# Kernel optimization log

Measured on AMD Instinct MI355X. Metric: run time of the kernel, lower is better.

Reference implementation:

```python
import jax, jax.numpy as jnp
import numpy as np

B, T, C, H = 2, 1024, 1024, 16
D = C // H                      # head_dim = 64
NG, BS = 64, 16                 # HBS groups / block_size (1024 = 64*16)
SQ = 32                         # sqrt_dim (1024 = 32*32)


def layer_norm(x, g, b, eps=1e-5):
    m = jnp.mean(x, axis=-1, keepdims=True)
    v = jnp.var(x, axis=-1, keepdims=True)
    return (x - m) * jax.lax.rsqrt(v + eps) * g + b


def hbs_proj(x, pre_g, pre_b, block_w, w_row, w_col, alpha, bias):
    # HierarchicalBlockShuffleLayer forward (dim=1024, no padding needed)
    xn = layer_norm(x, pre_g, pre_b)
    x_flat = xn.reshape(-1, C)
    # block mixing: per-group 16x16 matmul, then flip feature axis
    g = x_flat.reshape(-1, NG, BS)
    y_mixed = jnp.einsum('ngi,gij->ngj', g, block_w).reshape(-1, C)
    block_out = y_mixed[..., ::-1]
    # monarch branch: 32x32 grid, right-multiply W_col then W_row^T
    grid = x_flat.reshape(-1, SQ, SQ)
    z = jnp.einsum('nij,jc->nic', grid, w_col)
    z = jnp.einsum('nic,rc->nir', z, w_row).reshape(-1, C)
    out = block_out + alpha * z + bias
    return out.reshape(x.shape)


def setup_inputs() -> dict:
    key = jax.random.key(0)
    ks = jax.random.split(key, 12)
    inp = {
        'x': jax.random.normal(ks[0], (B, T, C), jnp.float32),
        'c_attn_w': jax.random.normal(ks[1], (3 * C, C), jnp.float32) * (1.0 / np.sqrt(C)),
        'c_attn_b': jnp.zeros((3 * C,), jnp.float32),
        'focus_gate': jnp.float32(0.0),
        'attn_norm_g': jnp.ones((D,), jnp.float32),
        'attn_norm_b': jnp.zeros((D,), jnp.float32),
        'out_norm_g': jnp.ones((C,), jnp.float32),
        'out_norm_b': jnp.zeros((C,), jnp.float32),
        'proj_pre_g': jnp.ones((C,), jnp.float32),
        'proj_pre_b': jnp.zeros((C,), jnp.float32),
        'proj_block_w': jax.random.normal(ks[2], (NG, BS, BS), jnp.float32) * 0.5 / np.sqrt(BS),
        'proj_w_row': jax.random.normal(ks[3], (SQ, SQ), jnp.float32) * 0.1 / np.sqrt(SQ),
        'proj_w_col': jax.random.normal(ks[4], (SQ, SQ), jnp.float32) * 0.1 / np.sqrt(SQ),
        'proj_alpha': jnp.float32(0.0),
        'proj_bias': jnp.zeros((C,), jnp.float32),
    }
    return inp


def reference(x, c_attn_w, c_attn_b, focus_gate, attn_norm_g, attn_norm_b,
              out_norm_g, out_norm_b, proj_pre_g, proj_pre_b, proj_block_w,
              proj_w_row, proj_w_col, proj_alpha, proj_bias):
    scale = 1.0 / np.sqrt(D)
    qkv = x @ c_attn_w.T + c_attn_b                      # [B,T,3C]
    q, k, v = jnp.split(qkv, 3, axis=2)
    # [B,H,T,D]
    q = q.reshape(B, T, H, D).transpose(0, 2, 1, 3)
    k = k.reshape(B, T, H, D).transpose(0, 2, 1, 3)
    v = v.reshape(B, T, H, D).transpose(0, 2, 1, 3)

    # --- causal linear attention branch (fp32) ---
    Qp = jax.nn.elu(q * scale) + 1.0
    Kp = jax.nn.elu(k * scale) + 1.0
    KV = jnp.einsum('bhtd,bhte->bhtde', Kp, v)           # [B,H,T,D,D]
    KV_cum = jnp.cumsum(KV, axis=2)
    K_cum = jnp.cumsum(Kp, axis=2)
    numer = jnp.einsum('bhtd,bhtde->bhte', Qp, KV_cum)
    denom = jnp.einsum('bhtd,bhtd->bht', Qp, K_cum)[..., None]
    y_lin = numer / (denom + 1e-4)                       # [B,H,T,D]
    y_lin = layer_norm(y_lin.transpose(0, 2, 1, 3), attn_norm_g, attn_norm_b)
    y_lin = y_lin.transpose(0, 2, 1, 3)

    # --- standard causal SDPA branch ---
    scores = jnp.einsum('bhqd,bhkd->bhqk', q, k) * scale
    causal = jnp.tril(jnp.ones((T, T), bool))
    scores = jnp.where(causal, scores, -jnp.inf)
    attn = jax.nn.softmax(scores, axis=-1)
    y_sharp = jnp.einsum('bhqk,bhkd->bhqd', attn, v)

    # --- gated combine + output projection ---
    alpha = jax.nn.sigmoid(focus_gate)
    y = alpha * y_sharp + (1.0 - alpha) * y_lin
    y = y.transpose(0, 2, 1, 3).reshape(B, T, C)
    y = layer_norm(y, out_norm_g, out_norm_b)
    return hbs_proj(y, proj_pre_g, proj_pre_b, proj_block_w,
                    proj_w_row, proj_w_col, proj_alpha, proj_bias)
```

## Files before the change

kernel.cpp:

```cpp
#include <hip/hip_runtime.h>
#include <math.h>

constexpr int T_ = 1024;
constexpr int C_ = 1024;
constexpr int H_ = 16;
constexpr int D_ = 64;
#define SCALE 0.125f

typedef unsigned short u16;
typedef __attribute__((ext_vector_type(8))) short short8;
typedef __attribute__((ext_vector_type(4))) float f32x4;

__device__ __forceinline__ float elu1(float x) { return x > 0.f ? x + 1.f : expf(x); }

__device__ __forceinline__ u16 f2bf(float f) {
    union { float f; unsigned u; } c; c.f = f;
    unsigned r = (c.u + 0x7fffu + ((c.u >> 16) & 1u)) >> 16;
    return (u16)r;
}
__device__ __forceinline__ float bf2f(u16 u) {
    union { unsigned u; float f; } c; c.u = (unsigned)u << 16;
    return c.f;
}

#define GLL16(g, l)                                                            \
    __builtin_amdgcn_global_load_lds(                                          \
        (const __attribute__((address_space(1))) void*)(g),                    \
        (__attribute__((address_space(3))) void*)(l), 16, 0, 0)

__global__ __launch_bounds__(256) void k0_cast(
    const float* __restrict__ s, u16* __restrict__ d, int n4)
{
    int i = blockIdx.x * 256 + threadIdx.x;
    if (i < n4) {
        float4 v = reinterpret_cast<const float4*>(s)[i];
        ushort4 o;
        o.x = f2bf(v.x); o.y = f2bf(v.y); o.z = f2bf(v.z); o.w = f2bf(v.w);
        reinterpret_cast<ushort4*>(d)[i] = o;
    }
}

__global__ __launch_bounds__(256) void k1_qkv(
    const u16* __restrict__ xbf, const u16* __restrict__ wbf,
    const float* __restrict__ bias,
    u16* __restrict__ qb, u16* __restrict__ kb, u16* __restrict__ vb)
{
    __shared__ __align__(16) u16 As[128 * 32];
    __shared__ __align__(16) u16 Bs[128 * 32];
    const int tid = threadIdx.x;
    const int wave = tid >> 6, lane = tid & 63;
    const int quad = lane >> 4, l15 = lane & 15;
    const int m0 = blockIdx.y << 7, n0 = blockIdx.x << 7;
    const int wm = (wave >> 1) << 6, wn = (wave & 1) << 6;

    const int rowS = (wave << 5) + (lane >> 2);
    const int seg8 = (lane & 3) << 3;
    const u16* gA1 = xbf + (size_t)(m0 + rowS) * 1024 + seg8;
    const u16* gA2 = gA1 + (size_t)16 * 1024;
    const u16* gB1 = wbf + (size_t)(n0 + rowS) * 1024 + seg8;
    const u16* gB2 = gB1 + (size_t)16 * 1024;
    u16* lA1 = &As[(wave << 5) * 32];
    u16* lA2 = lA1 + 16 * 32;
    u16* lB1 = &Bs[(wave << 5) * 32];
    u16* lB2 = lB1 + 16 * 32;

    f32x4 zero4 = {0.f, 0.f, 0.f, 0.f};
    f32x4 acc[4][4];
#pragma unroll
    for (int i = 0; i < 4; i++)
#pragma unroll
        for (int j = 0; j < 4; j++) acc[i][j] = zero4;

    for (int k0 = 0; k0 < 1024; k0 += 32) {
        GLL16(gA1 + k0, lA1);
        GLL16(gA2 + k0, lA2);
        GLL16(gB1 + k0, lB1);
        GLL16(gB2 + k0, lB2);
        __syncthreads();
        short8 a[4], b[4];
#pragma unroll
        for (int mi = 0; mi < 4; mi++)
            a[mi] = *(const short8*)&As[(wm + mi * 16 + l15) * 32 + (quad << 3)];
#pragma unroll
        for (int ni = 0; ni < 4; ni++)
            b[ni] = *(const short8*)&Bs[(wn + ni * 16 + l15) * 32 + (quad << 3)];
#pragma unroll
        for (int mi = 0; mi < 4; mi++)
#pragma unroll
            for (int ni = 0; ni < 4; ni++)
                acc[mi][ni] = __builtin_amdgcn_mfma_f32_16x16x32_bf16(
                    a[mi], b[ni], acc[mi][ni], 0, 0, 0);
        __syncthreads();
    }
#pragma unroll
    for (int ni = 0; ni < 4; ni++) {
        int n_g = n0 + wn + ni * 16 + l15;
        int which = n_g >> 10;
        int h = (n_g >> 6) & 15;
        int d = n_g & 63;
        u16* dst = (which == 0) ? qb : (which == 1) ? kb : vb;
        float bz = bias[n_g];
#pragma unroll
        for (int mi = 0; mi < 4; mi++) {
#pragma unroll
            for (int reg = 0; reg < 4; reg++) {
                int m = m0 + wm + mi * 16 + (quad << 2) + reg;
                int bi = m >> 10, t = m & 1023;
                dst[((size_t)(bi * 16 + h) << 16) + ((size_t)t << 6) + d] =
                    f2bf(acc[mi][ni][reg] + bz);
            }
        }
    }
}

__global__ __launch_bounds__(256) void k_vt(
    const u16* __restrict__ vb, u16* __restrict__ vtb)
{
    const int t0 = blockIdx.x << 6, bh = blockIdx.y;
    __shared__ __align__(16) u16 Vs[64][72];
    const int tid = threadIdx.x;
#pragma unroll
    for (int u = 0; u < 2; u++) {
        int idx = (tid + (u << 8)) << 3;
        int r = idx >> 6, c = idx & 63;
        *(uint4*)&Vs[r][c] =
            *(const uint4*)&vb[((size_t)bh << 16) + ((size_t)(t0 + r) << 6) + c];
    }
    __syncthreads();
#pragma unroll
    for (int u = 0; u < 2; u++) {
        int idx = (tid + (u << 8)) << 3;
        int dd = idx >> 6, c0 = idx & 63;
        union { u16 s[8]; uint4 v; } tmp;
#pragma unroll
        for (int j = 0; j < 8; j++) tmp.s[j] = Vs[c0 + j][dd];
        *(uint4*)&vtb[((size_t)((bh << 6) + dd) << 10) + t0 + c0] = tmp.v;
    }
}

__global__ __launch_bounds__(256) void k2a_chunkkv(
    const u16* __restrict__ kb, const u16* __restrict__ vb,
    float* __restrict__ Sg, float* __restrict__ svg)
{
    const int chunk = blockIdx.x, bh = blockIdx.y;
    const int t0 = chunk << 6;
    __shared__ float Ks[64][65];
    __shared__ float Vs[64][65];
    const int tid = threadIdx.x;
    const u16* kp = kb + (size_t)bh * T_ * D_;
    const u16* vp = vb + (size_t)bh * T_ * D_;
#pragma unroll
    for (int ii = 0; ii < 16; ii++) {
        int idx = tid + (ii << 8);
        int row = idx >> 6, col = idx & 63;
        Ks[row][col] = elu1(bf2f(kp[(size_t)(t0 + row) * D_ + col]) * SCALE);
        Vs[row][col] = bf2f(vp[(size_t)(t0 + row) * D_ + col]);
    }
    __syncthreads();
    const int tr = tid >> 4, tc = tid & 15;
    const int d0 = tr * 4, e0 = tc * 4;
    float acc[4][4] = {};
    for (int c = 0; c < 64; c++) {
        float a[4], b[4];
#pragma unroll
        for (int i = 0; i < 4; i++) a[i] = Ks[c][d0 + i];
#pragma unroll
        for (int j = 0; j < 4; j++) b[j] = Vs[c][e0 + j];
#pragma unroll
        for (int i = 0; i < 4; i++)
#pragma unroll
            for (int j = 0; j < 4; j++) acc[i][j] += a[i] * b[j];
    }
    float* so = Sg + ((size_t)bh * 16 + chunk) * 4096;
#pragma unroll
    for (int i = 0; i < 4; i++) {
        float4 o = {acc[i][0], acc[i][1], acc[i][2], acc[i][3]};
        *reinterpret_cast<float4*>(&so[(d0 + i) * 64 + e0]) = o;
    }
    if (tc == 0) {
#pragma unroll
        for (int i = 0; i < 4; i++) {
            float s = 0.f;
            for (int c = 0; c < 64; c++) s += Ks[c][d0 + i];
            svg[((size_t)bh * 16 + chunk) * 64 + d0 + i] = s;
        }
    }
}

__global__ __launch_bounds__(256) void k2s_scan(
    float* __restrict__ Sg, float* __restrict__ svg)
{
    int gid = blockIdx.x * 256 + threadIdx.x;
    if (gid < 131072) {
        int bh = gid >> 12, e = gid & 4095;
        float* base = Sg + ((size_t)bh << 16) + e;
        float v[16];
#pragma unroll
        for (int c = 0; c < 16; c++) v[c] = base[(size_t)c << 12];
        float run = 0.f;
#pragma unroll
        for (int c = 0; c < 16; c++) {
            base[(size_t)c << 12] = run;
            run += v[c];
        }
    } else if (gid < 131072 + 2048) {
        int g2 = gid - 131072;
        int bh = g2 >> 6, d = g2 & 63;
        float* base = svg + ((size_t)bh << 10) + d;
        float v[16];
#pragma unroll
        for (int c = 0; c < 16; c++) v[c] = base[c << 6];
        float run = 0.f;
#pragma unroll
        for (int c = 0; c < 16; c++) {
            base[c << 6] = run;
            run += v[c];
        }
    }
}

__global__ __launch_bounds__(256) void k2b_lin(
    const u16* __restrict__ qbp, const u16* __restrict__ kbp,
    const u16* __restrict__ vbp,
    const float* __restrict__ Sg, const float* __restrict__ svg,
    const float* __restrict__ ang, const float* __restrict__ anb,
    float* __restrict__ ylin)
{
    const int chunk = blockIdx.x, bh = blockIdx.y;
    const int t0 = chunk << 6;
    __shared__ __align__(16) float bufA[64][68];
    __shared__ float bufQ[64][65];
    __shared__ float bufK[64][65];
    __shared__ float svec[64];
    const int tid = threadIdx.x;
    const u16* qp = qbp + (size_t)bh * T_ * D_;
    const u16* kp = kbp + (size_t)bh * T_ * D_;
    const u16* vp = vbp + (size_t)bh * T_ * D_;
    const float* sp = Sg + (((size_t)bh * 16 + chunk) << 12);
#pragma unroll
    for (int u = 0; u < 4; u++) {
        int idx = (tid + (u << 8)) << 2;
        int dd = idx >> 6, e = idx & 63;
        *(float4*)&bufA[dd][e] = *(const float4*)&sp[idx];
    }
    if (tid < 64) svec[tid] = svg[(((size_t)bh * 16 + chunk) << 6) + tid];
#pragma unroll
    for (int ii = 0; ii < 16; ii++) {
        int idx = tid + (ii << 8);
        int row = idx >> 6, col = idx & 63;
        bufQ[col][row] = elu1(bf2f(qp[(size_t)(t0 + row) * D_ + col]) * SCALE);
    }
    __syncthreads();
    const int tr = tid >> 4, tc = tid & 15;
    const int r0 = tr * 4, c0 = tc * 4;
    float N[4][4] = {};
    float pden[4];
    for (int dd = 0; dd < 64; dd++) {
        float a[4], b[4];
#pragma unroll
        for (int i = 0; i < 4; i++) a[i] = bufQ[dd][r0 + i];
#pragma unroll
        for (int j = 0; j < 4; j++) b[j] = bufA[dd][c0 + j];
#pragma unroll
        for (int i = 0; i < 4; i++)
#pragma unroll
            for (int j = 0; j < 4; j++) N[i][j] += a[i] * b[j];
    }
#pragma unroll
    for (int i = 0; i < 4; i++) {
        float s = 0.f;
#pragma unroll
        for (int j = 0; j < 4; j++) s += bufQ[c0 + j][r0 + i] * svec[c0 + j];
        pden[i] = s;
    }
    __syncthreads();
#pragma unroll
    for (int ii = 0; ii < 16; ii++) {
        int idx = tid + (ii << 8);
        int row = idx >> 6, col = idx & 63;
        bufK[col][row] = elu1(bf2f(kp[(size_t)(t0 + row) * D_ + col]) * SCALE);
        bufA[row][col] = bf2f(vp[(size_t)(t0 + row) * D_ + col]);
    }
    __syncthreads();
    float sc[4][4] = {};
    for (int dd = 0; dd < 64; dd++) {
        float a[4], b[4];
#pragma unroll
        for (int i = 0; i < 4; i++) a[i] = bufQ[dd][r0 + i];
#pragma unroll
        for (int j = 0; j < 4; j++) b[j] = bufK[dd][c0 + j];
#pragma unroll
        for (int i = 0; i < 4; i++)
#pragma unroll
            for (int j = 0; j < 4; j++) sc[i][j] += a[i] * b[j];
    }
    __syncthreads();
#pragma unroll
    for (int i = 0; i < 4; i++) {
        float s = 0.f;
#pragma unroll
        for (int j = 0; j < 4; j++) {
            float pv = ((c0 + j) <= (r0 + i)) ? sc[i][j] : 0.f;
            bufQ[c0 + j][r0 + i] = pv;
            s += pv;
        }
        pden[i] += s;
    }
#pragma unroll
    for (int i = 0; i < 4; i++) {
#pragma unroll
        for (int off = 1; off < 16; off <<= 1)
            pden[i] += __shfl_xor(pden[i], off);
    }
    __syncthreads();
    for (int c = 0; c < 64; c++) {
        float a[4], b[4];
#pragma unroll
        for (int i = 0; i < 4; i++) a[i] = bufQ[c][r0 + i];
#pragma unroll
        for (int j = 0; j < 4; j++) b[j] = bufA[c][c0 + j];
#pragma unroll
        for (int i = 0; i < 4; i++)
#pragma unroll
            for (int j = 0; j < 4; j++) N[i][j] += a[i] * b[j];
    }
    float yv[4][4], s1[4], s2[4];
#pragma unroll
    for (int i = 0; i < 4; i++) {
        float inv = 1.f / (pden[i] + 1e-4f);
        s1[i] = 0.f; s2[i] = 0.f;
#pragma unroll
        for (int j = 0; j < 4; j++) {
            float t = N[i][j] * inv;
            yv[i][j] = t; s1[i] += t; s2[i] += t * t;
        }
    }
#pragma unroll
    for (int i = 0; i < 4; i++) {
#pragma unroll
        for (int off = 1; off < 16; off <<= 1) {
            s1[i] += __shfl_xor(s1[i], off);
            s2[i] += __shfl_xor(s2[i], off);
        }
    }
#pragma unroll
    for (int i = 0; i < 4; i++) {
        float mean = s1[i] * (1.f / 64.f);
        float var = s2[i] * (1.f / 64.f) - mean * mean;
        float rstd = rsqrtf(var + 1e-5f);
        float4 o;
        o.x = (yv[i][0] - mean) * rstd * ang[c0 + 0] + anb[c0 + 0];
        o.y = (yv[i][1] - mean) * rstd * ang[c0 + 1] + anb[c0 + 1];
        o.z = (yv[i][2] - mean) * rstd * ang[c0 + 2] + anb[c0 + 2];
        o.w = (yv[i][3] - mean) * rstd * ang[c0 + 3] + anb[c0 + 3];
        *reinterpret_cast<float4*>(
            &ylin[((size_t)bh * T_ + t0 + r0 + i) * D_ + c0]) = o;
    }
}

__global__ __launch_bounds__(256) void k3_sharp(
    const u16* __restrict__ qbp, const u16* __restrict__ kbp,
    const u16* __restrict__ vtb,
    const float* __restrict__ ylin, const float* __restrict__ fg,
    float* __restrict__ ycomb)
{
    const int bh = blockIdx.y;
    __shared__ __align__(16) u16 Qs[64][72];
    __shared__ __align__(16) u16 Ks[64][72];
    __shared__ __align__(16) u16 Vt[64][72];
    __shared__ __align__(16) u16 Pa[64][72];
    const int tid = threadIdx.x;
    const int wave = tid >> 6, lane = tid & 63;
    const int quad = lane >> 4, l15 = lane & 15;
    const float al = 1.f / (1.f + expf(-fg[0]));
    const int bi = bh >> 4, h = bh & 15;
    const f32x4 zero4 = {0.f, 0.f, 0.f, 0.f};

    for (int phase = 0; phase < 2; phase++) {
        const int qi = phase == 0 ? (int)blockIdx.x : 15 - (int)blockIdx.x;
        __syncthreads();
#pragma unroll
        for (int u = 0; u < 2; u++) {
            int idx = (tid + (u << 8)) << 3;
            int r = idx >> 6, c = idx & 63;
            *(uint4*)&Qs[r][c] = *(const uint4*)
                &qbp[((size_t)bh << 16) + ((size_t)((qi << 6) + r) << 6) + c];
        }
        __syncthreads();
        short8 bq[2];
        bq[0] = *(const short8*)&Qs[(wave << 4) + l15][(quad << 3)];
        bq[1] = *(const short8*)&Qs[(wave << 4) + l15][32 + (quad << 3)];
        f32x4 O[4];
#pragma unroll
        for (int dt = 0; dt < 4; dt++) O[dt] = zero4;
        float m_run = -INFINITY, l_run = 0.f;
        const int r_g = (qi << 6) + (wave << 4) + l15;

        for (int ki = 0; ki <= qi; ki++) {
            __syncthreads();
#pragma unroll
            for (int u = 0; u < 2; u++) {
                int idx = (tid + (u << 8)) << 3;
                int r = idx >> 6, c = idx & 63;
                *(uint4*)&Ks[r][c] = *(const uint4*)
                    &kbp[((size_t)bh << 16) + ((size_t)((ki << 6) + r) << 6) + c];
                *(uint4*)&Vt[r][c] = *(const uint4*)
                    &vtb[((size_t)((bh << 6) + r) << 10) + (ki << 6) + c];
            }
            __syncthreads();
            f32x4 st[4];
#pragma unroll
            for (int ct = 0; ct < 4; ct++) st[ct] = zero4;
#pragma unroll
            for (int ks = 0; ks < 2; ks++) {
#pragma unroll
                for (int ct = 0; ct < 4; ct++) {
                    short8 a = *(const short8*)
                        &Ks[(ct << 4) + l15][(ks << 5) + (quad << 3)];
                    st[ct] = __builtin_amdgcn_mfma_f32_16x16x32_bf16(
                        a, bq[ks], st[ct], 0, 0, 0);
                }
            }
            float mloc = -INFINITY;
#pragma unroll
            for (int ct = 0; ct < 4; ct++)
#pragma unroll
                for (int reg = 0; reg < 4; reg++) {
                    int c_g = (ki << 6) + (ct << 4) + (quad << 2) + reg;
                    float s = st[ct][reg] * SCALE;
                    if (c_g > r_g) s = -INFINITY;
                    st[ct][reg] = s;
                    mloc = fmaxf(mloc, s);
                }
            mloc = fmaxf(mloc, __shfl_xor(mloc, 16));
            mloc = fmaxf(mloc, __shfl_xor(mloc, 32));
            float mnew = fmaxf(m_run, mloc);
            float corr = __expf(m_run - mnew);
            m_run = mnew;
            float rsum = 0.f;
#pragma unroll
            for (int ct = 0; ct < 4; ct++) {
                u16 pk[4];
#pragma unroll
                for (int reg = 0; reg < 4; reg++) {
                    float pv = __expf(st[ct][reg] - mnew);
                    rsum += pv;
                    pk[reg] = f2bf(pv);
                }
                unsigned lo = (unsigned)pk[0] | ((unsigned)pk[1] << 16);
                unsigned hi = (unsigned)pk[2] | ((unsigned)pk[3] << 16);
                uint2 pkv; pkv.x = lo; pkv.y = hi;
                *(uint2*)&Pa[(wave << 4) + l15][(ct << 4) + (quad << 2)] = pkv;
            }
            rsum += __shfl_xor(rsum, 16);
            rsum += __shfl_xor(rsum, 32);
            l_run = l_run * corr + rsum;
            float co[4];
#pragma unroll
            for (int reg = 0; reg < 4; reg++)
                co[reg] = __shfl(corr, ((lane >> 4) << 2) + reg);
#pragma unroll
            for (int dt = 0; dt < 4; dt++)
#pragma unroll
                for (int reg = 0; reg < 4; reg++) O[dt][reg] *= co[reg];
#pragma unroll
            for (int ks = 0; ks < 2; ks++) {
                short8 ap = *(const short8*)
                    &Pa[(wave << 4) + l15][(ks << 5) + (quad << 3)];
#pragma unroll
                for (int dt = 0; dt < 4; dt++) {
                    short8 bv = *(const short8*)
                        &Vt[(dt << 4) + l15][(ks << 5) + (quad << 3)];
                    O[dt] = __builtin_amdgcn_mfma_f32_16x16x32_bf16(
                        ap, bv, O[dt], 0, 0, 0);
                }
            }
        }
        float lo4[4];
#pragma unroll
        for (int reg = 0; reg < 4; reg++)
            lo4[reg] = __shfl(l_run, ((lane >> 4) << 2) + reg);
#pragma unroll
        for (int reg = 0; reg < 4; reg++) {
            int t = (qi << 6) + (wave << 4) + (quad << 2) + reg;
            float inv = al / lo4[reg];
#pragma unroll
            for (int dt = 0; dt < 4; dt++) {
                int d = (dt << 4) + l15;
                float yl = ylin[(((size_t)bh << 10) + t) * 64 + d];
                ycomb[((size_t)((bi << 10) + t) << 10) + (h << 6) + d] =
                    O[dt][reg] * inv + (1.f - al) * yl;
            }
        }
    }
}

__global__ __launch_bounds__(256) void k4_proj(
    const float* __restrict__ ycomb,
    const float* __restrict__ og, const float* __restrict__ ob,
    const float* __restrict__ pg, const float* __restrict__ pb,
    const float* __restrict__ bw, const float* __restrict__ wrow,
    const float* __restrict__ wcol, const float* __restrict__ palpha,
    const float* __restrict__ pbias, float* __restrict__ out)
{
    const int tok = blockIdx.x;
    __shared__ float xb[1024];
    __shared__ float ymix[1024];
    __shared__ float zs[1024];
    __shared__ float red[8];
    const int tid = threadIdx.x;
    const int c0 = tid << 2;
    const float* yrow = ycomb + ((size_t)tok << 10);
    float4 v4 = *reinterpret_cast<const float4*>(yrow + c0);
    float v[4] = {v4.x, v4.y, v4.z, v4.w};
    float s1 = v[0] + v[1] + v[2] + v[3];
    float s2 = v[0]*v[0] + v[1]*v[1] + v[2]*v[2] + v[3]*v[3];
#pragma unroll
    for (int off = 1; off < 64; off <<= 1) {
        s1 += __shfl_xor(s1, off); s2 += __shfl_xor(s2, off);
    }
    if ((tid & 63) == 0) { red[(tid >> 6) * 2] = s1; red[(tid >> 6) * 2 + 1] = s2; }
    __syncthreads();
    s1 = red[0] + red[2] + red[4] + red[6];
    s2 = red[1] + red[3] + red[5] + red[7];
    __syncthreads();
    {
        float mean = s1 * (1.f / 1024.f);
        float var = s2 * (1.f / 1024.f) - mean * mean;
        float rstd = rsqrtf(var + 1e-5f);
#pragma unroll
        for (int q = 0; q < 4; q++)
            v[q] = (v[q] - mean) * rstd * og[c0 + q] + ob[c0 + q];
    }
    s1 = v[0] + v[1] + v[2] + v[3];
    s2 = v[0]*v[0] + v[1]*v[1] + v[2]*v[2] + v[3]*v[3];
#pragma unroll
    for (int off = 1; off < 64; off <<= 1) {
        s1 += __shfl_xor(s1, off); s2 += __shfl_xor(s2, off);
    }
    if ((tid & 63) == 0) { red[(tid >> 6) * 2] = s1; red[(tid >> 6) * 2 + 1] = s2; }
    __syncthreads();
    s1 = red[0] + red[2] + red[4] + red[6];
    s2 = red[1] + red[3] + red[5] + red[7];
    __syncthreads();
    {
        float mean = s1 * (1.f / 1024.f);
        float var = s2 * (1.f / 1024.f) - mean * mean;
        float rstd = rsqrtf(var + 1e-5f);
#pragma unroll
        for (int q = 0; q < 4; q++)
            xb[c0 + q] = (v[q] - mean) * rstd * pg[c0 + q] + pb[c0 + q];
    }
    __syncthreads();
    {
        int g = tid >> 2;
        int jb = (tid & 3) << 2;
        float acc[4] = {0.f, 0.f, 0.f, 0.f};
        const float* xg = &xb[g << 4];
        const float* bwg = &bw[g << 8];
        for (int i = 0; i < 16; i++) {
            float xv = xg[i];
#pragma unroll
            for (int q = 0; q < 4; q++) acc[q] += xv * bwg[i * 16 + jb + q];
        }
#pragma unroll
        for (int q = 0; q < 4; q++) ymix[(g << 4) + jb + q] = acc[q];
    }
    {
        int i_ = tid >> 3;
        int ccb = (tid << 2) & 31;
        float acc[4] = {0.f, 0.f, 0.f, 0.f};
        const float* xg = &xb[i_ << 5];
        for (int j = 0; j < 32; j++) {
            float xv = xg[j];
#pragma unroll
            for (int q = 0; q < 4; q++) acc[q] += xv * wcol[(j << 5) + ccb + q];
        }
#pragma unroll
        for (int q = 0; q < 4; q++) zs[(i_ << 5) + ccb + q] = acc[q];
    }
    __syncthreads();
    {
        int i_ = tid >> 3;
        int rb = (tid << 2) & 31;
        const float* z1row = &zs[i_ << 5];
        const float al = palpha[0];
        float vout[4];
#pragma unroll
        for (int q = 0; q < 4; q++) {
            float acc = 0.f;
            const float* wr = &wrow[(rb + q) << 5];
            for (int cc = 0; cc < 32; cc++) acc += z1row[cc] * wr[cc];
            int ch = (i_ << 5) + rb + q;
            vout[q] = ymix[1023 - ch] + al * acc + pbias[ch];
        }
        float4 o = {vout[0], vout[1], vout[2], vout[3]};
        *reinterpret_cast<float4*>(&out[((size_t)tok << 10) + (i_ << 5) + rb]) = o;
    }
}

extern "C" void kernel_launch(void* const* d_in, const int* in_sizes, int n_in,
                              void* d_out, int out_size, void* d_ws, size_t ws_size,
                              hipStream_t stream) {
    const float* x   = (const float*)d_in[0];
    const float* w   = (const float*)d_in[1];
    const float* wb  = (const float*)d_in[2];
    const float* fg  = (const float*)d_in[3];
    const float* ang = (const float*)d_in[4];
    const float* anb = (const float*)d_in[5];
    const float* ong = (const float*)d_in[6];
    const float* onb = (const float*)d_in[7];
    const float* ppg = (const float*)d_in[8];
    const float* ppb = (const float*)d_in[9];
    const float* pbw = (const float*)d_in[10];
    const float* pwr = (const float*)d_in[11];
    const float* pwc = (const float*)d_in[12];
    const float* pal = (const float*)d_in[13];
    const float* pbi = (const float*)d_in[14];

    uint8_t* p = (uint8_t*)d_ws;
    u16* xbf = (u16*)p;  p += (size_t)2048 * 1024 * 2;
    u16* wbf = (u16*)p;  p += (size_t)3072 * 1024 * 2;
    u16* qb  = (u16*)p;  p += (size_t)32 * 1024 * 64 * 2;
    u16* kb  = (u16*)p;  p += (size_t)32 * 1024 * 64 * 2;
    u16* vb  = (u16*)p;  p += (size_t)32 * 1024 * 64 * 2;
    u16* vtb = (u16*)p;  p += (size_t)32 * 1024 * 64 * 2;
    float* ylin  = (float*)p;  p += (size_t)32 * 1024 * 64 * 4;
    float* ycomb = (float*)p;  p += (size_t)32 * 1024 * 64 * 4;
    float* Sg    = (float*)p;  p += (size_t)32 * 16 * 4096 * 4;
    float* svg   = (float*)p;  p += (size_t)32 * 16 * 64 * 4;
    float* out   = (float*)d_out;

    k0_cast<<<2048, 256, 0, stream>>>(x, xbf, 524288);
    k0_cast<<<3072, 256, 0, stream>>>(w, wbf, 786432);
    k1_qkv<<<dim3(24, 16), 256, 0, stream>>>(xbf, wbf, wb, qb, kb, vb);
    k_vt<<<dim3(16, 32), 256, 0, stream>>>(vb, vtb);
    k2a_chunkkv<<<dim3(16, 32), 256, 0, stream>>>(kb, vb, Sg, svg);
    k2s_scan<<<521, 256, 0, stream>>>(Sg, svg);
    k2b_lin<<<dim3(16, 32), 256, 0, stream>>>(qb, kb, vb, Sg, svg, ang, anb, ylin);
    k3_sharp<<<dim3(8, 32), 256, 0, stream>>>(qb, kb, vtb, ylin, fg, ycomb);
    k4_proj<<<2048, 256, 0, stream>>>(ycomb, ong, onb, ppg, ppb, pbw, pwr, pwc, pal, pbi, out);
}
```

Before: 247.5 us.

## Precompute combined monarch matrix and fuse projection branches without shared staging

Adds a tiny kernel that computes M = alpha * W_col * W_row^T once (a 32x32 matrix). The projection kernel then does one 32-term dot product per output instead of two chained matmuls through shared memory. The flip is handled by having each thread compute the block-mix outputs that map to its own output channels, which removes the ymix/zs shared buffers and two barriers. Weights are read with float4 loads. The cost is an extra tiny launch and a change in float summation order.

```diff
diff --git a/kernel.cpp b/kernel.cpp
--- a/kernel.cpp
+++ b/kernel.cpp
@@ -495,18 +495,32 @@
     }
 }
 
+__global__ __launch_bounds__(256) void k4m(
+    const float* __restrict__ wcol, const float* __restrict__ wrow,
+    const float* __restrict__ palpha, float* __restrict__ Mg)
+{
+    const int tid = threadIdx.x;
+    const int j = tid >> 3, r0 = (tid & 7) << 2;
+    const float al = palpha[0];
+    float acc[4] = {0.f, 0.f, 0.f, 0.f};
+    for (int c = 0; c < 32; c++) {
+        float wc = wcol[(j << 5) + c];
+#pragma unroll
+        for (int q = 0; q < 4; q++) acc[q] += wc * wrow[((r0 + q) << 5) + c];
+    }
+    float4 o = {al * acc[0], al * acc[1], al * acc[2], al * acc[3]};
+    *reinterpret_cast<float4*>(&Mg[(j << 5) + r0]) = o;
+}
+
 __global__ __launch_bounds__(256) void k4_proj(
     const float* __restrict__ ycomb,
     const float* __restrict__ og, const float* __restrict__ ob,
     const float* __restrict__ pg, const float* __restrict__ pb,
-    const float* __restrict__ bw, const float* __restrict__ wrow,
-    const float* __restrict__ wcol, const float* __restrict__ palpha,
+    const float* __restrict__ bw, const float* __restrict__ Mg,
     const float* __restrict__ pbias, float* __restrict__ out)
 {
     const int tok = blockIdx.x;
     __shared__ float xb[1024];
-    __shared__ float ymix[1024];
-    __shared__ float zs[1024];
     __shared__ float red[8];
     const int tid = threadIdx.x;
     const int c0 = tid << 2;
@@ -542,7 +556,6 @@
     __syncthreads();
     s1 = red[0] + red[2] + red[4] + red[6];
     s2 = red[1] + red[3] + red[5] + red[7];
-    __syncthreads();
     {
         float mean = s1 * (1.f / 1024.f);
         float var = s2 * (1.f / 1024.f) - mean * mean;
@@ -552,51 +565,39 @@
             xb[c0 + q] = (v[q] - mean) * rstd * pg[c0 + q] + pb[c0 + q];
     }
     __syncthreads();
+    const int g = tid >> 2;
+    const int jb = (tid & 3) << 2;
+    float acc[4] = {0.f, 0.f, 0.f, 0.f};
     {
-        int g = tid >> 2;
-        int jb = (tid & 3) << 2;
-        float acc[4] = {0.f, 0.f, 0.f, 0.f};
         const float* xg = &xb[g << 4];
-        const float* bwg = &bw[g << 8];
+        const float* bwg = &bw[(g << 8) + jb];
         for (int i = 0; i < 16; i++) {
             float xv = xg[i];
-#pragma unroll
-            for (int q = 0; q < 4; q++) acc[q] += xv * bwg[i * 16 + jb + q];
-        }
-#pragma unroll
-        for (int q = 0; q < 4; q++) ymix[(g << 4) + jb + q] = acc[q];
-    }
+            float4 wv = *reinterpret_cast<const float4*>(&bwg[i << 4]);
+            acc[0] += xv * wv.x; acc[1] += xv * wv.y;
+            acc[2] += xv * wv.z; acc[3] += xv * wv.w;
+        }
+    }
+    const int C0 = ((63 - g) << 4) + 12 - jb;
+    const int i2 = C0 >> 5, r0 = C0 & 31;
+    float z2[4] = {0.f, 0.f, 0.f, 0.f};
     {
-        int i_ = tid >> 3;
-        int ccb = (tid << 2) & 31;
-        float acc[4] = {0.f, 0.f, 0.f, 0.f};
-        const float* xg = &xb[i_ << 5];
+        const float* xg = &xb[i2 << 5];
+        const float* mg = &Mg[r0];
         for (int j = 0; j < 32; j++) {
             float xv = xg[j];
-#pragma unroll
-            for (int q = 0; q < 4; q++) acc[q] += xv * wcol[(j << 5) + ccb + q];
-        }
-#pragma unroll
-        for (int q = 0; q < 4; q++) zs[(i_ << 5) + ccb + q] = acc[q];
-    }
-    __syncthreads();
-    {
-        int i_ = tid >> 3;
-        int rb = (tid << 2) & 31;
-        const float* z1row = &zs[i_ << 5];
-        const float al = palpha[0];
-        float vout[4];
-#pragma unroll
-        for (int q = 0; q < 4; q++) {
-            float acc = 0.f;
-            const float* wr = &wrow[(rb + q) << 5];
-            for (int cc = 0; cc < 32; cc++) acc += z1row[cc] * wr[cc];
-            int ch = (i_ << 5) + rb + q;
-            vout[q] = ymix[1023 - ch] + al * acc + pbias[ch];
-        }
-        float4 o = {vout[0], vout[1], vout[2], vout[3]};
-        *reinterpret_cast<float4*>(&out[((size_t)tok << 10) + (i_ << 5) + rb]) = o;
-    }
+            float4 mv = *reinterpret_cast<const float4*>(&mg[j << 5]);
+            z2[0] += xv * mv.x; z2[1] += xv * mv.y;
+            z2[2] += xv * mv.z; z2[3] += xv * mv.w;
+        }
+    }
+    float4 bz = *reinterpret_cast<const float4*>(&pbias[C0]);
+    float4 o;
+    o.x = acc[3] + z2[0] + bz.x;
+    o.y = acc[2] + z2[1] + bz.y;
+    o.z = acc[1] + z2[2] + bz.z;
+    o.w = acc[0] + z2[3] + bz.w;
+    *reinterpret_cast<float4*>(&out[((size_t)tok << 10) + C0]) = o;
 }
 
 extern "C" void kernel_launch(void* const* d_in, const int* in_sizes, int n_in,
@@ -629,15 +630,17 @@
     float* ycomb = (float*)p;  p += (size_t)32 * 1024 * 64 * 4;
     float* Sg    = (float*)p;  p += (size_t)32 * 16 * 4096 * 4;
     float* svg   = (float*)p;  p += (size_t)32 * 16 * 64 * 4;
+    float* Mg    = (float*)p;  p += (size_t)32 * 32 * 4;
     float* out   = (float*)d_out;
 
     k0_cast<<<2048, 256, 0, stream>>>(x, xbf, 524288);
     k0_cast<<<3072, 256, 0, stream>>>(w, wbf, 786432);
+    k4m<<<1, 256, 0, stream>>>(pwc, pwr, pal, Mg);
     k1_qkv<<<dim3(24, 16), 256, 0, stream>>>(xbf, wbf, wb, qb, kb, vb);
     k_vt<<<dim3(16, 32), 256, 0, stream>>>(vb, vtb);
     k2a_chunkkv<<<dim3(16, 32), 256, 0, stream>>>(kb, vb, Sg, svg);
     k2s_scan<<<521, 256, 0, stream>>>(Sg, svg);
     k2b_lin<<<dim3(16, 32), 256, 0, stream>>>(qb, kb, vb, Sg, svg, ang, anb, ylin);
     k3_sharp<<<dim3(8, 32), 256, 0, stream>>>(qb, kb, vtb, ylin, fg, ycomb);
-    k4_proj<<<2048, 256, 0, stream>>>(ycomb, ong, onb, ppg, ppb, pbw, pwr, pwc, pal, pbi, out);
-}
+    k4_proj<<<2048, 256, 0, stream>>>(ycomb, ong, onb, ppg, ppb, pbw, Mg, pbi, out);
+}
```

Measured after the change: 225.5 us. -8.9%, faster.
